# Optimization experiments

Measured on AMD Instinct MI355X. Metric: run time of the kernel, lower is better.

## Reference

```python
import jax, jax.numpy as jnp
import numpy as np
from jax import lax

NUM_CHARS = 97
NUM_TAGS = 17
CHAR_DIM = 128
NF = 64
KS = (3, 5, 7)
HID = 128
B, S = 128, 512
NEG = -1e9


def setup_inputs() -> dict:
    key = jax.random.key(0)
    ks = iter(jax.random.split(key, 64))
    def nrm(shape, scale):
        return jax.random.normal(next(ks), shape, jnp.float32) * np.float32(scale)
    x = jax.random.randint(next(ks), (B, S), 1, NUM_CHARS)   # avoid padding id 0
    tags = jax.random.randint(next(ks), (B, S), 0, NUM_TAGS)
    mask = jnp.ones((B, S), jnp.float32)
    D = NF * len(KS)  # 192
    inp = dict(x=x, tags=tags, mask=mask)
    inp["emb"] = nrm((NUM_CHARS, CHAR_DIM), 0.1).at[0].set(0.0)  # padding_idx=0
    for k in KS:
        inp[f"cw{k}"] = nrm((NF, CHAR_DIM, k), 1.0 / np.sqrt(CHAR_DIM * k))
        inp[f"cb{k}"] = jnp.zeros((NF,), jnp.float32)
    inp["hw_w"] = nrm((D, D), 1.0 / np.sqrt(D)); inp["hw_b"] = jnp.zeros((D,), jnp.float32)
    inp["hwg_w"] = nrm((D, D), 1.0 / np.sqrt(D)); inp["hwg_b"] = jnp.zeros((D,), jnp.float32)
    for l, din in ((0, D), (1, 2 * HID)):
        for d in "fb":
            inp[f"wih{l}{d}"] = nrm((4 * HID, din), 1.0 / np.sqrt(din))
            inp[f"whh{l}{d}"] = nrm((4 * HID, HID), 1.0 / np.sqrt(HID))
            inp[f"b{l}{d}"] = jnp.zeros((4 * HID,), jnp.float32)  # b_ih + b_hh fused
    inp["cls_w"] = nrm((NUM_TAGS, 2 * HID), 1.0 / np.sqrt(2 * HID))
    inp["cls_b"] = jnp.zeros((NUM_TAGS,), jnp.float32)
    inp["trans"] = nrm((NUM_TAGS, NUM_TAGS), 0.1)
    inp["start_t"] = jnp.zeros((NUM_TAGS,), jnp.float32)
    inp["end_t"] = jnp.zeros((NUM_TAGS,), jnp.float32)
    return inp


def _conv1d(xc, w, b):
    # xc: [B, C, S], w: [O, C, k], 'same' padding for odd k (torch padding=k//2)
    k = w.shape[-1]
    out = lax.conv_general_dilated(xc, w, (1,), [(k // 2, k // 2)],
                                   dimension_numbers=("NCH", "OIH", "NCH"))
    return out + b[None, :, None]


def _lstm_dir(xseq, wih, whh, b, reverse):
    # xseq: [S, B, din] -> hidden outputs [S, B, HID]; torch gate order i,f,g,o
    xg = jnp.einsum("sbi,gi->sbg", xseq, wih) + b  # [S, B, 4H]
    h0 = jnp.zeros((xseq.shape[1], HID), xseq.dtype)
    def step(carry, g):
        h, c = carry
        z = g + h @ whh.T
        i, f, gg, o = jnp.split(z, 4, axis=-1)
        c = jax.nn.sigmoid(f) * c + jax.nn.sigmoid(i) * jnp.tanh(gg)
        h = jax.nn.sigmoid(o) * jnp.tanh(c)
        return (h, c), h
    _, hs = lax.scan(step, (h0, h0), xg, reverse=reverse)
    return hs


def _emissions(x, emb, cw3, cb3, cw5, cb5, cw7, cb7, hw_w, hw_b, hwg_w, hwg_b,
               wih0f, whh0f, b0f, wih0b, whh0b, b0b,
               wih1f, whh1f, b1f, wih1b, whh1b, b1b, cls_w, cls_b):
    char_mask = (x != 0).astype(jnp.float32)
    xc = emb[x].transpose(0, 2, 1)  # [B, C, S]
    h = jnp.concatenate([jax.nn.relu(_conv1d(xc, w, b))
                         for w, b in ((cw3, cb3), (cw5, cb5), (cw7, cb7))], axis=1)
    h = h.transpose(0, 2, 1)  # [B, S, 192]
    t = jax.nn.sigmoid(h @ hwg_w.T + hwg_b)
    hw = t * jax.nn.relu(h @ hw_w.T + hw_b) + (1.0 - t) * h  # highway
    seq = hw.transpose(1, 0, 2)  # [S, B, D]
    out0 = jnp.concatenate([_lstm_dir(seq, wih0f, whh0f, b0f, False),
                            _lstm_dir(seq, wih0b, whh0b, b0b, True)], axis=-1)
    out1 = jnp.concatenate([_lstm_dir(out0, wih1f, whh1f, b1f, False),
                            _lstm_dir(out0, wih1b, whh1b, b1b, True)], axis=-1)
    em = out1.transpose(1, 0, 2) @ cls_w.T + cls_b  # [B, S, T] (dropout: eval identity)
    m = char_mask[..., None]
    return em * m + (1.0 - m) * NEG


def _crf_loss(emissions, tags, mask, trans, start_t, end_t):
    bsz = emissions.shape[0]
    bi = jnp.arange(bsz)
    # gold path score (fully vectorized over time)
    em_sc = jnp.take_along_axis(emissions, tags[..., None], axis=2)[..., 0]  # [B,S]
    tr_sc = trans[tags[:, :-1], tags[:, 1:]]                                  # [B,S-1]
    score = start_t[tags[:, 0]] + em_sc[:, 0] + jnp.sum((tr_sc + em_sc[:, 1:]) * mask[:, 1:], axis=1)
    last_real = mask.sum(axis=1).astype(jnp.int32) - 1
    last_tag = tags[bi, jnp.maximum(last_real, 0)]
    score = score + end_t[last_tag] * (last_real >= 0).astype(jnp.float32)
    # log normalizer: forward DP over 17-tag state space via scan
    alpha0 = start_t + emissions[:, 0]
    def step(alpha, inp):
        em_i, m_i = inp
        nxt = jax.scipy.special.logsumexp(alpha[:, :, None] + trans[None], axis=1) + em_i
        return nxt * m_i[:, None] + alpha * (1.0 - m_i[:, None]), None
    alpha, _ = lax.scan(step, alpha0, (emissions[:, 1:].transpose(1, 0, 2), mask[:, 1:].T))
    logZ = jax.scipy.special.logsumexp(alpha + end_t, axis=1)
    return -(score - logZ).mean()


def reference(x, tags, mask, emb, cw3, cb3, cw5, cb5, cw7, cb7, hw_w, hw_b, hwg_w, hwg_b,
              wih0f, whh0f, b0f, wih0b, whh0b, b0b,
              wih1f, whh1f, b1f, wih1b, whh1b, b1b,
              cls_w, cls_b, trans, start_t, end_t):
    em = _emissions(x, emb, cw3, cb3, cw5, cb5, cw7, cb7, hw_w, hw_b, hwg_w, hwg_b,
                    wih0f, whh0f, b0f, wih0b, whh0b, b0b,
                    wih1f, whh1f, b1f, wih1b, whh1b, b1b, cls_w, cls_b)
    return _crf_loss(em, tags, mask, trans, start_t, end_t)
```

## Files before the change

### kernel.cpp

```cpp
#include <hip/hip_runtime.h>
#include <hip/hip_bf16.h>
#include <cstdint>
#include <cstddef>

namespace {

constexpr int kB = 128;
constexpr int kS = 512;
constexpr int kM = kB * kS;

typedef __hip_bfloat16 bf16;
typedef __attribute__((ext_vector_type(8))) short short8;
typedef __attribute__((ext_vector_type(4))) float f32x4;
typedef __attribute__((ext_vector_type(4))) unsigned int u32x4;

__device__ __forceinline__ float sig_(float x) {
  return __builtin_amdgcn_rcpf(1.f + __expf(-x));
}
__device__ __forceinline__ float tanh_(float x) {
  return 1.f - 2.f * __builtin_amdgcn_rcpf(__expf(2.f * x) + 1.f);
}
__device__ __forceinline__ float b2f(bf16 h) { return __bfloat162float(h); }
__device__ __forceinline__ bf16 f2b(float f) { return __float2bfloat16(f); }

__device__ __forceinline__ void unpack8(uint4 v, float* o) {
  o[0] = __uint_as_float(v.x << 16); o[1] = __uint_as_float(v.x & 0xffff0000u);
  o[2] = __uint_as_float(v.y << 16); o[3] = __uint_as_float(v.y & 0xffff0000u);
  o[4] = __uint_as_float(v.z << 16); o[5] = __uint_as_float(v.z & 0xffff0000u);
  o[6] = __uint_as_float(v.w << 16); o[7] = __uint_as_float(v.w & 0xffff0000u);
}

__device__ __forceinline__ void gl_lds16(const void* g, void* l) {
  __builtin_amdgcn_global_load_lds((const __attribute__((address_space(1))) void*)g,
                                   (__attribute__((address_space(3))) void*)l, 16, 0, 0);
}

__device__ __forceinline__ void fast_barrier() {
  __builtin_amdgcn_sched_barrier(0);
  asm volatile("s_waitcnt lgkmcnt(0)" ::: "memory");
  __builtin_amdgcn_s_barrier();
  __builtin_amdgcn_sched_barrier(0);
}

__global__ void k_wprep(const float* __restrict__ wih0f, const float* __restrict__ wih0b,
                        const float* __restrict__ wih1f, const float* __restrict__ wih1b,
                        const float* __restrict__ hw_w, const float* __restrict__ hwg_w,
                        const float* __restrict__ whh0f, const float* __restrict__ whh0b,
                        const float* __restrict__ whh1f, const float* __restrict__ whh1b,
                        bf16* __restrict__ W0b, bf16* __restrict__ W1b,
                        bf16* __restrict__ WAb, bf16* __restrict__ WGb,
                        bf16* __restrict__ WHb) {
  int b = blockIdx.x, t = threadIdx.x;
  if (b < 768) {
    const float* s = (b < 384) ? wih0f : wih0b;
    bf16* d = W0b + (b < 384 ? 0 : 98304);
    int i = (b & 383) * 256 + t;
    int n = i / 192, k = i - n * 192;
    d[i] = f2b(s[((n & 3) * 128 + (n >> 2)) * 192 + k]);
  } else if (b < 1792) {
    int bb = b - 768;
    const float* s = (bb < 512) ? wih1f : wih1b;
    bf16* d = W1b + (bb < 512 ? 0 : 131072);
    int i = (bb & 511) * 256 + t;
    int n = i >> 8, k = i & 255;
    d[i] = f2b(s[((n & 3) * 128 + (n >> 2)) * 256 + k]);
  } else if (b < 2080) {
    int bb = b - 1792;
    const float* s = (bb < 144) ? hw_w : hwg_w;
    bf16* d = (bb < 144) ? WAb : WGb;
    int i = (bb % 144) * 256 + t;
    d[i] = f2b(s[i]);
  } else {
    int bb = b - 2080;
    int which = bb >> 8;
    const float* s = (which == 0) ? whh0f : (which == 1) ? whh0b : (which == 2) ? whh1f : whh1b;
    int i = (bb & 255) * 256 + t;
    WHb[which * 65536 + i] = f2b(s[i]);
  }
}

__global__ void k_table(const float* __restrict__ emb,
                        const float* __restrict__ cw3,
                        const float* __restrict__ cw5,
                        const float* __restrict__ cw7,
                        float* __restrict__ tbl) {
  int e = blockIdx.x;
  int tap = e / 97, ch = e % 97;
  int f = threadIdx.x;
  const float* w; int kk, dk;
  if (tap < 3)      { w = cw3; kk = 3; dk = tap; }
  else if (tap < 8) { w = cw5; kk = 5; dk = tap - 3; }
  else              { w = cw7; kk = 7; dk = tap - 8; }
  const float* er = emb + ch * 128;
  float s = 0.f;
  for (int c = 0; c < 128; ++c) s = fmaf(er[c], w[(f * 128 + c) * kk + dk], s);
  tbl[(size_t)e * 64 + f] = s;
}

__global__ void k_conv(const int* __restrict__ x, const float* __restrict__ tbl,
                       const float* __restrict__ cb3, const float* __restrict__ cb5,
                       const float* __restrict__ cb7, bf16* __restrict__ outA) {
  __shared__ int chs[70];
  int b = blockIdx.x >> 3;
  int s0 = (blockIdx.x & 7) << 6;
  int tid = threadIdx.x;
  if (tid < 70) {
    int g = s0 - 3 + tid;
    chs[tid] = (g >= 0 && g < kS) ? x[b * kS + g] : 0;
  }
  __syncthreads();
  int wv = tid >> 6;
  int f = tid & 63;
  int ntap, tap0, half; const float* cb;
  if (wv == 0)      { ntap = 3; tap0 = 0; half = 1; cb = cb3; }
  else if (wv == 1) { ntap = 5; tap0 = 3; half = 2; cb = cb5; }
  else              { ntap = 7; tap0 = 8; half = 3; cb = cb7; }
  float bias = cb[f];
  for (int p = 0; p < 64; ++p) {
    float acc = bias;
    for (int dk = 0; dk < ntap; ++dk) {
      int c = chs[p + 3 - half + dk];
      acc += tbl[(size_t)((tap0 + dk) * 97 + c) * 64 + f];
    }
    outA[(size_t)(b * kS + s0 + p) * 192 + wv * 64 + f] = f2b(fmaxf(acc, 0.f));
  }
}

__global__ __launch_bounds__(256) void k_hw(
    const bf16* __restrict__ A,
    const bf16* __restrict__ Wa, const float* __restrict__ Ba,
    const bf16* __restrict__ Wg, const float* __restrict__ Bg,
    bf16* __restrict__ outB) {
  __shared__ __align__(16) short As[128 * 64];
  __shared__ __align__(16) short Was[64 * 64];
  __shared__ __align__(16) short Wgs[64 * 64];
  constexpr int K = 192;
  int tid = threadIdx.x;
  int w = tid >> 6, l = tid & 63;
  int m0 = blockIdx.x * 128, n0 = blockIdx.y * 64;
  int wr = w >> 1, wc = w & 1;
  int lr = l >> 3, lc = l & 7;
  f32x4 accA[4][2], accG[4][2];
#pragma unroll
  for (int i = 0; i < 4; ++i)
#pragma unroll
    for (int j = 0; j < 2; ++j) { accA[i][j] = (f32x4)0.f; accG[i][j] = (f32x4)0.f; }

  for (int kc = 0; kc < K; kc += 64) {
    __syncthreads();
#pragma unroll
    for (int i = 0; i < 4; ++i) {
      int r = w * 32 + i * 8;
      gl_lds16(A + (size_t)(m0 + r + lr) * K + kc + lc * 8, &As[r * 64]);
    }
#pragma unroll
    for (int i = 0; i < 2; ++i) {
      int r = w * 16 + i * 8;
      gl_lds16(Wa + (size_t)(n0 + r + lr) * K + kc + lc * 8, &Was[r * 64]);
      gl_lds16(Wg + (size_t)(n0 + r + lr) * K + kc + lc * 8, &Wgs[r * 64]);
    }
    __syncthreads();
#pragma unroll
    for (int kf = 0; kf < 2; ++kf) {
      short8 af[4], ba[2], bg[2];
#pragma unroll
      for (int mt = 0; mt < 4; ++mt)
        af[mt] = *(const short8*)&As[(wr * 64 + mt * 16 + (l & 15)) * 64 + kf * 32 + (l >> 4) * 8];
#pragma unroll
      for (int nt = 0; nt < 2; ++nt) {
        int rn = (wc * 32 + nt * 16 + (l & 15)) * 64 + kf * 32 + (l >> 4) * 8;
        ba[nt] = *(const short8*)&Was[rn];
        bg[nt] = *(const short8*)&Wgs[rn];
      }
#pragma unroll
      for (int mt = 0; mt < 4; ++mt)
#pragma unroll
        for (int nt = 0; nt < 2; ++nt) {
          accA[mt][nt] = __builtin_amdgcn_mfma_f32_16x16x32_bf16(af[mt], ba[nt], accA[mt][nt], 0, 0, 0);
          accG[mt][nt] = __builtin_amdgcn_mfma_f32_16x16x32_bf16(af[mt], bg[nt], accG[mt][nt], 0, 0, 0);
        }
    }
  }
#pragma unroll
  for (int nt = 0; nt < 2; ++nt) {
    int n = n0 + wc * 32 + nt * 16 + (l & 15);
    float bav = Ba[n], bgv = Bg[n];
#pragma unroll
    for (int mt = 0; mt < 4; ++mt) {
      int mb = m0 + wr * 64 + mt * 16 + (l >> 4) * 4;
#pragma unroll
      for (int r = 0; r < 4; ++r) {
        float av = accA[mt][nt][r] + bav;
        float gv = accG[mt][nt][r] + bgv;
        float tt = sig_(gv);
        float orig = b2f(A[(size_t)(mb + r) * K + n]);
        outB[(size_t)(mb + r) * K + n] = f2b(tt * fmaxf(av, 0.f) + (1.f - tt) * orig);
      }
    }
  }
}

__global__ __launch_bounds__(256) void k_pgemm(
    const bf16* __restrict__ A, int K,
    const bf16* __restrict__ W,
    const float* __restrict__ bfw, const float* __restrict__ bbw,
    bf16* __restrict__ xg) {
  __shared__ __align__(16) short As[128 * 64];
  __shared__ __align__(16) short Bs[128 * 64];
  int tid = threadIdx.x;
  int w = tid >> 6, l = tid & 63;
  int m0 = blockIdx.x * 128, n0 = blockIdx.y * 128;
  int wr = w >> 1, wc = w & 1;
  int lr = l >> 3, lc = l & 7;
  f32x4 acc[4][4];
#pragma unroll
  for (int i = 0; i < 4; ++i)
#pragma unroll
    for (int j = 0; j < 4; ++j) acc[i][j] = (f32x4)0.f;

  for (int kc = 0; kc < K; kc += 64) {
    __syncthreads();
#pragma unroll
    for (int i = 0; i < 4; ++i) {
      int r = w * 32 + i * 8;
      gl_lds16(A + (size_t)(m0 + r + lr) * K + kc + lc * 8, &As[r * 64]);
      gl_lds16(W + (size_t)(n0 + r + lr) * K + kc + lc * 8, &Bs[r * 64]);
    }
    __syncthreads();
#pragma unroll
    for (int kf = 0; kf < 2; ++kf) {
      short8 af[4], bfr[4];
#pragma unroll
      for (int mt = 0; mt < 4; ++mt)
        af[mt] = *(const short8*)&As[(wr * 64 + mt * 16 + (l & 15)) * 64 + kf * 32 + (l >> 4) * 8];
#pragma unroll
      for (int nt = 0; nt < 4; ++nt)
        bfr[nt] = *(const short8*)&Bs[(wc * 64 + nt * 16 + (l & 15)) * 64 + kf * 32 + (l >> 4) * 8];
#pragma unroll
      for (int mt = 0; mt < 4; ++mt)
#pragma unroll
        for (int nt = 0; nt < 4; ++nt)
          acc[mt][nt] = __builtin_amdgcn_mfma_f32_16x16x32_bf16(af[mt], bfr[nt], acc[mt][nt], 0, 0, 0);
    }
  }
#pragma unroll
  for (int nt = 0; nt < 4; ++nt) {
    int n = n0 + wc * 64 + nt * 16 + (l & 15);
    int nn = n & 511;
    float bv = ((n < 512) ? bfw : bbw)[(nn & 3) * 128 + (nn >> 2)];
#pragma unroll
    for (int mt = 0; mt < 4; ++mt) {
      int mb = m0 + wr * 64 + mt * 16 + (l >> 4) * 4;
#pragma unroll
      for (int r = 0; r < 4; ++r) {
        int row = mb + r;
        int rp = ((row & 511) << 7) | (row >> 9);
        xg[((size_t)rp << 10) + n] = f2b(acc[mt][nt][r] + bv);
      }
    }
  }
}

__global__ __attribute__((amdgpu_waves_per_eu(2, 2))) __launch_bounds__(512)
void k_rec5(
    const bf16* __restrict__ xg,
    const bf16* __restrict__ whhF, const bf16* __restrict__ whhB,
    bf16* __restrict__ out) {
  constexpr int HS = 160;
  int blk = blockIdx.x;
  int dir = blk >> 5;
  int seq0 = (blk & 31) * 4;
  const short* whhs = (const short*)(dir ? whhB : whhF);
  const bool rev = (dir == 1);
  int tid = threadIdx.x;
  int w = tid >> 6, l = tid & 63;
  int ln = l & 15, lk = l >> 4;
  int s = l & 3;
  int r = (l >> 2) & 3;
  int u = w * 16 + lk * 4 + r;
  int seq = seq0 + s;

  u32x4 wfu[4][4];
#pragma unroll
  for (int g = 0; g < 4; ++g)
#pragma unroll
    for (int kk = 0; kk < 4; ++kk) {
      wfu[g][kk] = *(const u32x4*)&whhs[(size_t)(g * 128 + w * 16 + ln) * 128 + kk * 32 + lk * 8];
      asm volatile("" : "+v"(wfu[g][kk]));
    }

  __shared__ __align__(16) short HT[2][4][HS];
  for (int i = tid; i < 2 * 4 * HS; i += 512) ((short*)HT)[i] = 0;

  float c = 0.f;

  const bf16* xbase = xg + (size_t)seq * 1024 + dir * 512 + u * 4;
  bf16* obase = out + (size_t)seq * 131072 + (size_t)dir * 128 + u;

  uint2 xA, xB;
  {
    int p0 = rev ? 511 : 0, p1 = rev ? 510 : 1;
    xA = *(const uint2*)(xbase + ((size_t)p0 << 17));
    xB = *(const uint2*)(xbase + ((size_t)p1 << 17));
  }
  __syncthreads();

  auto do_step = [&](int tphys, int tpref, const short* RB, short* WB, uint2& x) {
    short8 b0 = *(const short8*)&RB[s * HS + 0  + lk * 8];
    short8 b1 = *(const short8*)&RB[s * HS + 32 + lk * 8];
    short8 b2 = *(const short8*)&RB[s * HS + 64 + lk * 8];
    short8 b3 = *(const short8*)&RB[s * HS + 96 + lk * 8];
    uint2 xc = x;
    x = *(const uint2*)(xbase + ((size_t)tpref << 17));
    f32x4 alo[4], ahi[4];
#pragma unroll
    for (int g = 0; g < 4; ++g) {
      alo[g] = __builtin_amdgcn_mfma_f32_16x16x32_bf16(
          __builtin_bit_cast(short8, wfu[g][0]), b0, (f32x4)0.f, 0, 0, 0);
      ahi[g] = __builtin_amdgcn_mfma_f32_16x16x32_bf16(
          __builtin_bit_cast(short8, wfu[g][2]), b2, (f32x4)0.f, 0, 0, 0);
    }
#pragma unroll
    for (int g = 0; g < 4; ++g) {
      alo[g] = __builtin_amdgcn_mfma_f32_16x16x32_bf16(
          __builtin_bit_cast(short8, wfu[g][1]), b1, alo[g], 0, 0, 0);
      ahi[g] = __builtin_amdgcn_mfma_f32_16x16x32_bf16(
          __builtin_bit_cast(short8, wfu[g][3]), b3, ahi[g], 0, 0, 0);
    }
    float z[4];
#pragma unroll
    for (int g = 0; g < 4; ++g) {
      f32x4 a = alo[g] + ahi[g];
      float v01 = (r & 1) ? a[1] : a[0];
      float v23 = (r & 1) ? a[3] : a[2];
      z[g] = (r & 2) ? v23 : v01;
    }
    float xi = __uint_as_float(xc.x << 16);
    float xf = __uint_as_float(xc.x & 0xffff0000u);
    float xm = __uint_as_float(xc.y << 16);
    float xo = __uint_as_float(xc.y & 0xffff0000u);
    float ig = sig_(z[0] + xi), fg = sig_(z[1] + xf);
    float gv = tanh_(z[2] + xm), og = sig_(z[3] + xo);
    c = fmaf(fg, c, ig * gv);
    float h = og * tanh_(c);
    bf16 hb = f2b(h);
    *(short*)&WB[s * HS + u] = *(short*)&hb;
    *(bf16*)(obase + (size_t)tphys * 256) = hb;
  };

  for (int t = 0; t < kS; t += 2) {
    int ta = rev ? 511 - t : t;
    int tb = rev ? 510 - t : t + 1;
    int pa = (t + 2 < kS) ? t + 2 : kS - 1;
    int pb = (t + 3 < kS) ? t + 3 : kS - 1;
    int tpa = rev ? 511 - pa : pa;
    int tpb = rev ? 511 - pb : pb;
    do_step(ta, tpa, &HT[0][0][0], &HT[1][0][0], xA);
    fast_barrier();
    do_step(tb, tpb, &HT[1][0][0], &HT[0][0][0], xB);
    fast_barrier();
  }
}

__global__ __launch_bounds__(256) void k_cls(
    const bf16* __restrict__ out1, const float* __restrict__ cls_w,
    const float* __restrict__ cls_b, const int* __restrict__ x,
    float* __restrict__ em) {
  __shared__ float W[17 * 256];
  __shared__ float part[64 * 4 * 17];
  int tid = threadIdx.x;
  for (int i = tid; i < 17 * 256; i += 256) W[i] = cls_w[i];
  __syncthreads();
  int r = tid >> 2, q = tid & 3;
  size_t row = (size_t)blockIdx.x * 64 + r;
  float acc[17];
#pragma unroll
  for (int j = 0; j < 17; ++j) acc[j] = 0.f;
  const uint4* a4p = (const uint4*)(out1 + row * 256 + q * 64);
  for (int i = 0; i < 8; ++i) {
    float f8[8]; unpack8(a4p[i], f8);
#pragma unroll
    for (int j = 0; j < 17; ++j) {
      const float* wr = &W[j * 256 + q * 64 + i * 8];
#pragma unroll
      for (int e = 0; e < 8; ++e) acc[j] = fmaf(f8[e], wr[e], acc[j]);
    }
  }
#pragma unroll
  for (int j = 0; j < 17; ++j) part[(r * 4 + q) * 17 + j] = acc[j];
  __syncthreads();
  for (int idx = tid; idx < 64 * 17; idx += 256) {
    int rr = idx / 17, j = idx % 17;
    size_t row2 = (size_t)blockIdx.x * 64 + rr;
    float v = part[(rr * 4 + 0) * 17 + j] + part[(rr * 4 + 1) * 17 + j] +
              part[(rr * 4 + 2) * 17 + j] + part[(rr * 4 + 3) * 17 + j] + cls_b[j];
    em[row2 * 17 + j] = (x[row2] != 0) ? v : -1e9f;
  }
}

__global__ __launch_bounds__(64) void k_crf(
    const float* __restrict__ em, const int* __restrict__ tags,
    const float* __restrict__ mask, const float* __restrict__ trans,
    const float* __restrict__ start_t, const float* __restrict__ end_t,
    float* __restrict__ res) {
  int b = blockIdx.x;
  int lane = threadIdx.x;
  const float* emB = em + (size_t)b * kS * 17;
  const int* tg = tags + b * kS;
  const float* mk = mask + b * kS;

  float tcol[17];
  if (lane < 17) {
#pragma unroll
    for (int i = 0; i < 17; ++i) tcol[i] = trans[i * 17 + lane];
  }
  float sc = 0.f, msum = 0.f;
  for (int t = lane; t < kS; t += 64) msum += mk[t];
  for (int t = 1 + lane; t < kS; t += 64)
    sc += (trans[tg[t - 1] * 17 + tg[t]] + emB[(size_t)t * 17 + tg[t]]) * mk[t];
#pragma unroll
  for (int o = 32; o; o >>= 1) { sc += __shfl_xor(sc, o); msum += __shfl_xor(msum, o); }

  __shared__ float al[17];
  if (lane < 17) al[lane] = start_t[lane] + emB[lane];
  __syncthreads();
  for (int t = 1; t < kS; ++t) {
    float nxt = 0.f;
    if (lane < 17) {
      float v[17]; float mx = -3.4e38f;
#pragma unroll
      for (int i = 0; i < 17; ++i) { v[i] = al[i] + tcol[i]; mx = fmaxf(mx, v[i]); }
      float s = 0.f;
#pragma unroll
      for (int i = 0; i < 17; ++i) s += __expf(v[i] - mx);
      float m = mk[t];
      nxt = (mx + __logf(s) + emB[(size_t)t * 17 + lane]) * m + al[lane] * (1.f - m);
    }
    __syncthreads();
    if (lane < 17) al[lane] = nxt;
    __syncthreads();
  }
  float val = (lane < 17) ? al[lane] + end_t[lane] : -3.4e38f;
  float mx = val;
#pragma unroll
  for (int o = 32; o; o >>= 1) mx = fmaxf(mx, __shfl_xor(mx, o));
  float s = (lane < 17) ? __expf(val - mx) : 0.f;
#pragma unroll
  for (int o = 32; o; o >>= 1) s += __shfl_xor(s, o);
  float logZ = mx + __logf(s);
  if (lane == 0) {
    float score = sc + start_t[tg[0]] + emB[tg[0]];
    int last_real = (int)(msum + 0.5f) - 1;
    if (last_real >= 0) score += end_t[tg[last_real]];
    res[b] = logZ - score;
  }
}

__global__ void k_loss(const float* __restrict__ res, float* __restrict__ out) {
  __shared__ float s[128];
  int tid = threadIdx.x;
  s[tid] = res[tid];
  __syncthreads();
  for (int off = 64; off; off >>= 1) {
    if (tid < off) s[tid] += s[tid + off];
    __syncthreads();
  }
  if (tid == 0) out[0] = s[0] / 128.f;
}

}

extern "C" void kernel_launch(void* const* d_in, const int* in_sizes, int n_in,
                              void* d_out, int out_size, void* d_ws, size_t ws_size,
                              hipStream_t stream) {
  (void)in_sizes; (void)n_in; (void)out_size; (void)ws_size;
  const int*   x       = (const int*)  d_in[0];
  const int*   tags    = (const int*)  d_in[1];
  const float* mask    = (const float*)d_in[2];
  const float* emb     = (const float*)d_in[3];
  const float* cw3     = (const float*)d_in[4];
  const float* cb3     = (const float*)d_in[5];
  const float* cw5     = (const float*)d_in[6];
  const float* cb5     = (const float*)d_in[7];
  const float* cw7     = (const float*)d_in[8];
  const float* cb7     = (const float*)d_in[9];
  const float* hw_w    = (const float*)d_in[10];
  const float* hw_b    = (const float*)d_in[11];
  const float* hwg_w   = (const float*)d_in[12];
  const float* hwg_b   = (const float*)d_in[13];
  const float* wih0f   = (const float*)d_in[14];
  const float* whh0f   = (const float*)d_in[15];
  const float* b0f     = (const float*)d_in[16];
  const float* wih0b   = (const float*)d_in[17];
  const float* whh0b   = (const float*)d_in[18];
  const float* b0b     = (const float*)d_in[19];
  const float* wih1f   = (const float*)d_in[20];
  const float* whh1f   = (const float*)d_in[21];
  const float* b1f     = (const float*)d_in[22];
  const float* wih1b   = (const float*)d_in[23];
  const float* whh1b   = (const float*)d_in[24];
  const float* b1b     = (const float*)d_in[25];
  const float* cls_w   = (const float*)d_in[26];
  const float* cls_b   = (const float*)d_in[27];
  const float* trans   = (const float*)d_in[28];
  const float* start_t = (const float*)d_in[29];
  const float* end_t   = (const float*)d_in[30];

  char* ws = (char*)d_ws;
  const size_t OFF_W0 = 393216;
  const size_t OFF_W1 = OFF_W0 + (size_t)1024 * 192 * 2;
  const size_t OFF_WA = OFF_W1 + (size_t)1024 * 256 * 2;
  const size_t OFF_WG = OFF_WA + (size_t)192 * 192 * 2;
  const size_t OFF_WH = OFF_WG + (size_t)192 * 192 * 2;
  const size_t OFF_A  = OFF_WH + (size_t)4 * 512 * 128 * 2;
  const size_t SZ_A   = (size_t)kM * 192 * 2;
  const size_t OFF_B  = OFF_A + SZ_A;
  const size_t OFF_O0 = OFF_B + SZ_A;
  const size_t OFF_XG = OFF_O0 + (size_t)kM * 256 * 2;
  float* tbl  = (float*)ws;
  bf16*  W0b  = (bf16*)(ws + OFF_W0);
  bf16*  W1b  = (bf16*)(ws + OFF_W1);
  bf16*  WAb  = (bf16*)(ws + OFF_WA);
  bf16*  WGb  = (bf16*)(ws + OFF_WG);
  bf16*  WHb  = (bf16*)(ws + OFF_WH);
  bf16*  bufA = (bf16*)(ws + OFF_A);
  bf16*  bufB = (bf16*)(ws + OFF_B);
  bf16*  out0 = (bf16*)(ws + OFF_O0);
  bf16*  out1 = (bf16*)(ws + OFF_A);
  bf16*  xg   = (bf16*)(ws + OFF_XG);
  float* em   = (float*)(ws + OFF_O0);
  float* resv = (float*)(ws + OFF_O0 + (size_t)kM * 17 * 4);

  k_wprep<<<3104, 256, 0, stream>>>(wih0f, wih0b, wih1f, wih1b, hw_w, hwg_w,
                                    whh0f, whh0b, whh1f, whh1b,
                                    W0b, W1b, WAb, WGb, WHb);

  k_table<<<15 * 97, 64, 0, stream>>>(emb, cw3, cw5, cw7, tbl);
  k_conv<<<kB * (kS / 64), 192, 0, stream>>>(x, tbl, cb3, cb5, cb7, bufA);
  k_hw<<<dim3(kM / 128, 3), 256, 0, stream>>>(bufA, WAb, hw_b, WGb, hwg_b, bufB);

  k_pgemm<<<dim3(kM / 128, 8), 256, 0, stream>>>(bufB, 192, W0b, b0f, b0b, xg);
  k_rec5<<<64, 512, 0, stream>>>(xg, WHb + 0 * 65536, WHb + 1 * 65536, out0);
  k_pgemm<<<dim3(kM / 128, 8), 256, 0, stream>>>(out0, 256, W1b, b1f, b1b, xg);
  k_rec5<<<64, 512, 0, stream>>>(xg, WHb + 2 * 65536, WHb + 3 * 65536, out1);

  k_cls<<<kM / 64, 256, 0, stream>>>(out1, cls_w, cls_b, x, em);
  k_crf<<<kB, 64, 0, stream>>>(em, tags, mask, trans, start_t, end_t, resv);
  k_loss<<<1, 128, 0, stream>>>(resv, (float*)d_out);
}
```

Before: 1.081 ms.

## Split LSTM recurrence across 128 blocks with 2 sequences and 4 waves each

The recurrent LSTM kernel now runs 128 blocks of 256 threads instead of 64 blocks of 512. Each block handles 2 sequences per direction instead of 4, and each wave owns 32 hidden units, holding twice as many W_hh fragments in registers. The goal is to spread the latency-bound serial recurrence over more CUs and shrink per-block barrier cost. In exchange, each wave issues twice the MFMAs per step in a serial accumulation chain, and register pressure is higher.

```diff
diff --git a/kernel.cpp b/kernel.cpp
--- a/kernel.cpp
+++ b/kernel.cpp
@@ -261,36 +261,40 @@
   }
 }
 
-__global__ __attribute__((amdgpu_waves_per_eu(2, 2))) __launch_bounds__(512)
-void k_rec5(
+__global__ __attribute__((amdgpu_waves_per_eu(1, 1))) __launch_bounds__(256)
+void k_rec6(
     const bf16* __restrict__ xg,
     const bf16* __restrict__ whhF, const bf16* __restrict__ whhB,
     bf16* __restrict__ out) {
   constexpr int HS = 160;
   int blk = blockIdx.x;
-  int dir = blk >> 5;
-  int seq0 = (blk & 31) * 4;
+  int dir = blk >> 6;
+  int seq0 = (blk & 63) * 2;
   const short* whhs = (const short*)(dir ? whhB : whhF);
   const bool rev = (dir == 1);
   int tid = threadIdx.x;
   int w = tid >> 6, l = tid & 63;
   int ln = l & 15, lk = l >> 4;
-  int s = l & 3;
+  int s = l & 1;
+  int ut = (l >> 1) & 1;
   int r = (l >> 2) & 3;
-  int u = w * 16 + lk * 4 + r;
+  int ul = ut * 16 + lk * 4 + r;
+  int u = w * 32 + ul;
   int seq = seq0 + s;
 
-  u32x4 wfu[4][4];
+  u32x4 wfu[4][2][4];
 #pragma unroll
   for (int g = 0; g < 4; ++g)
 #pragma unroll
-    for (int kk = 0; kk < 4; ++kk) {
-      wfu[g][kk] = *(const u32x4*)&whhs[(size_t)(g * 128 + w * 16 + ln) * 128 + kk * 32 + lk * 8];
-      asm volatile("" : "+v"(wfu[g][kk]));
-    }
-
-  __shared__ __align__(16) short HT[2][4][HS];
-  for (int i = tid; i < 2 * 4 * HS; i += 512) ((short*)HT)[i] = 0;
+    for (int t2 = 0; t2 < 2; ++t2)
+#pragma unroll
+      for (int kk = 0; kk < 4; ++kk) {
+        wfu[g][t2][kk] = *(const u32x4*)&whhs[(size_t)(g * 128 + w * 32 + t2 * 16 + ln) * 128 + kk * 32 + lk * 8];
+        asm volatile("" : "+v"(wfu[g][t2][kk]));
+      }
+
+  __shared__ __align__(16) short HT[2][2][HS];
+  for (int i = tid; i < 2 * 2 * HS; i += 256) ((short*)HT)[i] = 0;
 
   float c = 0.f;
 
@@ -312,28 +316,33 @@
     short8 b3 = *(const short8*)&RB[s * HS + 96 + lk * 8];
     uint2 xc = x;
     x = *(const uint2*)(xbase + ((size_t)tpref << 17));
-    f32x4 alo[4], ahi[4];
+    f32x4 acc[4][2];
+#pragma unroll
+    for (int g = 0; g < 4; ++g) { acc[g][0] = (f32x4)0.f; acc[g][1] = (f32x4)0.f; }
+#pragma unroll
+    for (int g = 0; g < 4; ++g)
+#pragma unroll
+      for (int t2 = 0; t2 < 2; ++t2) {
+        acc[g][t2] = __builtin_amdgcn_mfma_f32_16x16x32_bf16(
+            __builtin_bit_cast(short8, wfu[g][t2][0]), b0, acc[g][t2], 0, 0, 0);
+        acc[g][t2] = __builtin_amdgcn_mfma_f32_16x16x32_bf16(
+            __builtin_bit_cast(short8, wfu[g][t2][1]), b1, acc[g][t2], 0, 0, 0);
+        acc[g][t2] = __builtin_amdgcn_mfma_f32_16x16x32_bf16(
+            __builtin_bit_cast(short8, wfu[g][t2][2]), b2, acc[g][t2], 0, 0, 0);
+        acc[g][t2] = __builtin_amdgcn_mfma_f32_16x16x32_bf16(
+            __builtin_bit_cast(short8, wfu[g][t2][3]), b3, acc[g][t2], 0, 0, 0);
+      }
+    float z[4];
 #pragma unroll
     for (int g = 0; g < 4; ++g) {
-      alo[g] = __builtin_amdgcn_mfma_f32_16x16x32_bf16(
-          __builtin_bit_cast(short8, wfu[g][0]), b0, (f32x4)0.f, 0, 0, 0);
-      ahi[g] = __builtin_amdgcn_mfma_f32_16x16x32_bf16(
-          __builtin_bit_cast(short8, wfu[g][2]), b2, (f32x4)0.f, 0, 0, 0);
-    }
-#pragma unroll
-    for (int g = 0; g < 4; ++g) {
-      alo[g] = __builtin_amdgcn_mfma_f32_16x16x32_bf16(
-          __builtin_bit_cast(short8, wfu[g][1]), b1, alo[g], 0, 0, 0);
-      ahi[g] = __builtin_amdgcn_mfma_f32_16x16x32_bf16(
-          __builtin_bit_cast(short8, wfu[g][3]), b3, ahi[g], 0, 0, 0);
-    }
-    float z[4];
-#pragma unroll
-    for (int g = 0; g < 4; ++g) {
-      f32x4 a = alo[g] + ahi[g];
-      float v01 = (r & 1) ? a[1] : a[0];
-      float v23 = (r & 1) ? a[3] : a[2];
-      z[g] = (r & 2) ? v23 : v01;
+      f32x4 a0 = acc[g][0], a1 = acc[g][1];
+      float p01 = (r & 1) ? a0[1] : a0[0];
+      float p23 = (r & 1) ? a0[3] : a0[2];
+      float v0 = (r & 2) ? p23 : p01;
+      float q01 = (r & 1) ? a1[1] : a1[0];
+      float q23 = (r & 1) ? a1[3] : a1[2];
+      float v1 = (r & 2) ? q23 : q01;
+      z[g] = ut ? v1 : v0;
     }
     float xi = __uint_as_float(xc.x << 16);
     float xf = __uint_as_float(xc.x & 0xffff0000u);
@@ -540,9 +549,9 @@
   k_hw<<<dim3(kM / 128, 3), 256, 0, stream>>>(bufA, WAb, hw_b, WGb, hwg_b, bufB);
 
   k_pgemm<<<dim3(kM / 128, 8), 256, 0, stream>>>(bufB, 192, W0b, b0f, b0b, xg);
-  k_rec5<<<64, 512, 0, stream>>>(xg, WHb + 0 * 65536, WHb + 1 * 65536, out0);
+  k_rec6<<<128, 256, 0, stream>>>(xg, WHb + 0 * 65536, WHb + 1 * 65536, out0);
   k_pgemm<<<dim3(kM / 128, 8), 256, 0, stream>>>(out0, 256, W1b, b1f, b1b, xg);
-  k_rec5<<<64, 512, 0, stream>>>(xg, WHb + 2 * 65536, WHb + 3 * 65536, out1);
+  k_rec6<<<128, 256, 0, stream>>>(xg, WHb + 2 * 65536, WHb + 3 * 65536, out1);
 
   k_cls<<<kM / 64, 256, 0, stream>>>(out1, cls_w, cls_b, x, em);
   k_crf<<<kB, 64, 0, stream>>>(em, tags, mask, trans, start_t, end_t, resv);
```

After: 1.001 ms. 7.4% less time.
